# Optimization experiments

Hardware: AMD Instinct MI355X
Metric: run time of the kernel (lower is better)

## Reference

```python
import jax, jax.numpy as jnp
import numpy as np

# sparse displacement set used by UFlow's CostVolume (53 of the 9x9=81 offsets)
INDEX = [0, 2, 4, 6, 8, 10, 12, 14, 16, 18, 20, 21, 22, 23, 24, 26, 28, 29, 30, 31, 32, 33, 34, 36, 38, 39, 40, 41, 42, 44, 46, 47, 48, 49, 50, 51, 52, 54, 56, 57, 58, 59, 60, 62, 64, 66, 68, 70, 72, 74, 76, 78, 80]
MD = 4            # max_displacement
K = 2 * MD + 1    # 9


def setup_inputs() -> dict:
    key = jax.random.key(0)
    k1, k2 = jax.random.split(key)
    N, C, H, W = 8, 64, 160, 320
    in1 = jax.random.normal(k1, (N, C, H, W), dtype=jnp.float32)
    in2 = jax.random.normal(k2, (N, C, H, W), dtype=jnp.float32)
    return {"in1": in1, "in2": in2}


def reference(in1, in2):
    # one-hot kernels, padding=MD) shifts each repeated copy of in1 by a
    # displacement (dy, dx) = (idx//K - MD, idx%K - MD); multiply by repeated
    # in2; conv2 (grouped ones/dim kernel, kernel_size=1) averages over the
    # dim channels within each displacement group.
    # Equivalent fused form: out[:, j] = mean_c( shift(in1, off_j) * in2 ).
    n, c, h, w = in2.shape
    padded = jnp.pad(in1, ((0, 0), (0, 0), (MD, MD), (MD, MD)))  # zero-pad like conv padding
    outs = []
    for idx in INDEX:
        dy, dx = idx // K, idx % K  # static slice offsets into padded map
        shifted = padded[:, :, dy:dy + h, dx:dx + w]  # [n,c,h,w]
        outs.append(jnp.mean(shifted * in2, axis=1))  # [n,h,w]
    return jnp.stack(outs, axis=1)  # [n, 53, h, w]
```

## Files before the change

kernel.cpp:

```cpp
#include <hip/hip_runtime.h>


#define HH 160
#define WW 320
#define CHN 64
#define ND 53

__global__ __launch_bounds__(256)
void cost_volume_simple(const float* __restrict__ in1,
                        const float* __restrict__ in2,
                        float* __restrict__ out) {
    const int g = blockIdx.x * 256 + threadIdx.x;
    const int x = g % WW;
    const int y = (g / WW) % HH;
    const int n = g / (WW * HH);

    float acc[ND];
    #pragma unroll
    for (int d = 0; d < ND; ++d) acc[d] = 0.f;

    const float* base1 = in1 + (size_t)n * CHN * HH * WW;
    const float* base2 = in2 + (size_t)n * CHN * HH * WW;

    for (int c = 0; c < CHN; ++c) {
        const float v2 = base2[(size_t)c * HH * WW + y * WW + x];
        const float* pl = base1 + (size_t)c * HH * WW;

        float f[9];
        #define ROWLOAD(DY) { \
            const int yy = y + (DY) - 4; \
            const bool rowok = (yy >= 0) && (yy < HH); \
            const float* rp = pl + yy * WW + (x - 4); \
            _Pragma("unroll") \
            for (int j = 0; j < 9; ++j) { \
                const int xx = x + j - 4; \
                f[j] = (rowok && (xx >= 0) && (xx < WW)) ? rp[j] : 0.f; \
            } }
        #define ACC(D, J) acc[D] = fmaf(f[J], v2, acc[D]);

        ROWLOAD(0) ACC(0,0)  ACC(1,2)  ACC(2,4)  ACC(3,6)  ACC(4,8)
        ROWLOAD(1) ACC(5,1)  ACC(6,3)  ACC(7,5)  ACC(8,7)
        ROWLOAD(2) ACC(9,0)  ACC(10,2) ACC(11,3) ACC(12,4) ACC(13,5) ACC(14,6) ACC(15,8)
        ROWLOAD(3) ACC(16,1) ACC(17,2) ACC(18,3) ACC(19,4) ACC(20,5) ACC(21,6) ACC(22,7)
        ROWLOAD(4) ACC(23,0) ACC(24,2) ACC(25,3) ACC(26,4) ACC(27,5) ACC(28,6) ACC(29,8)
        ROWLOAD(5) ACC(30,1) ACC(31,2) ACC(32,3) ACC(33,4) ACC(34,5) ACC(35,6) ACC(36,7)
        ROWLOAD(6) ACC(37,0) ACC(38,2) ACC(39,3) ACC(40,4) ACC(41,5) ACC(42,6) ACC(43,8)
        ROWLOAD(7) ACC(44,1) ACC(45,3) ACC(46,5) ACC(47,7)
        ROWLOAD(8) ACC(48,0) ACC(49,2) ACC(50,4) ACC(51,6) ACC(52,8)
        #undef ROWLOAD
        #undef ACC
    }

    const float s = 1.0f / 64.0f;
    const size_t ob = (size_t)n * ND * HH * WW + (size_t)y * WW + x;
    #pragma unroll
    for (int d = 0; d < ND; ++d)
        out[ob + (size_t)d * HH * WW] = acc[d] * s;
}

extern "C" void kernel_launch(void* const* d_in, const int* in_sizes, int n_in,
                              void* d_out, int out_size, void* d_ws, size_t ws_size,
                              hipStream_t stream) {
    const float* in1 = (const float*)d_in[0];
    const float* in2 = (const float*)d_in[1];
    float* out = (float*)d_out;

    const int total = 8 * HH * WW;
    dim3 grid(total / 256);
    dim3 block(256);
    cost_volume_simple<<<grid, block, 0, stream>>>(in1, in2, out);
}
```

Before: 437.8 us.

## Compute four adjacent pixels per thread with float4 loads and deferred boundary masking

Each thread now produces four horizontally adjacent outputs, loading three float4 vectors per row so the 12 neighbouring values are shared across the four pixels, and stores results as float4. Boundary checks move out of the inner loop: loads are clamped to valid addresses, and out-of-range displacements are zeroed in the epilogue instead. Blocks shrink to 64 threads, and the block index is swizzled across the image. The intent is fewer load instructions, better vectorised memory access and less per-iteration branching. In exchange, 53 float4 accumulators (212 floats) raise register pressure and may spill or limit occupancy.

After: 643.4 us. 47.0% more time.

```diff
diff --git a/kernel.cpp b/kernel.cpp
--- a/kernel.cpp
+++ b/kernel.cpp
@@ -5,38 +5,58 @@
 #define WW 320
 #define CHN 64
 #define ND 53
+#define HW4 (HH * WW * 4)
+#define ROW4 (WW * 4)
+#define IMG4 (CHN * HW4)
+#define SIZEB (8 * IMG4)
+#define OIMG4 (ND * HW4)
 
-__global__ __launch_bounds__(256)
-void cost_volume_simple(const float* __restrict__ in1,
-                        const float* __restrict__ in2,
-                        float* __restrict__ out) {
-    const int g = blockIdx.x * 256 + threadIdx.x;
-    const int x = g % WW;
-    const int y = (g / WW) % HH;
-    const int n = g / (WW * HH);
+__global__ __launch_bounds__(64, 2)
+void cost_volume_x4(const float* __restrict__ in1,
+                    const float* __restrict__ in2,
+                    float* __restrict__ out) {
+    const int bid = blockIdx.x;
+    const int sb  = (bid & 7) * 200 + (bid >> 3);
+    const int g   = sb * 64 + threadIdx.x;
 
-    float acc[ND];
+    const int xg = g % 80;
+    const int x0 = xg * 4;
+    const int y  = (g / 80) % HH;
+    const int n  = g / (80 * HH);
+
+    const char* p1 = (const char*)in1;
+    const char* p2 = (const char*)in2;
+
+    float4 acc[ND];
     #pragma unroll
-    for (int d = 0; d < ND; ++d) acc[d] = 0.f;
+    for (int d = 0; d < ND; ++d) acc[d] = make_float4(0.f, 0.f, 0.f, 0.f);
 
-    const float* base1 = in1 + (size_t)n * CHN * HH * WW;
-    const float* base2 = in2 + (size_t)n * CHN * HH * WW;
+    int pc = n * IMG4 + x0 * 4 - 16;
+    int i2 = n * IMG4 + (y * WW + x0) * 4;
 
+    #pragma unroll 1
     for (int c = 0; c < CHN; ++c) {
-        const float v2 = base2[(size_t)c * HH * WW + y * WW + x];
-        const float* pl = base1 + (size_t)c * HH * WW;
+        const float4 w = *(const float4*)(p2 + i2);
+        float f[12];
 
-        float f[9];
         #define ROWLOAD(DY) { \
-            const int yy = y + (DY) - 4; \
-            const bool rowok = (yy >= 0) && (yy < HH); \
-            const float* rp = pl + yy * WW + (x - 4); \
-            _Pragma("unroll") \
-            for (int j = 0; j < 9; ++j) { \
-                const int xx = x + j - 4; \
-                f[j] = (rowok && (xx >= 0) && (xx < WW)) ? rp[j] : 0.f; \
-            } }
-        #define ACC(D, J) acc[D] = fmaf(f[J], v2, acc[D]);
+            int yy = y + (DY) - 4; \
+            yy = yy < 0 ? 0 : (yy > HH - 1 ? HH - 1 : yy); \
+            const int off = pc + yy * ROW4; \
+            const int o0 = off < 0 ? 0 : off; \
+            const int o2 = (off + 32 > SIZEB - 16) ? (SIZEB - 16) : (off + 32); \
+            const float4 a  = *(const float4*)(p1 + o0); \
+            const float4 b  = *(const float4*)(p1 + off + 16); \
+            const float4 cc = *(const float4*)(p1 + o2); \
+            f[0] = a.x;  f[1] = a.y;  f[2]  = a.z;  f[3]  = a.w; \
+            f[4] = b.x;  f[5] = b.y;  f[6]  = b.z;  f[7]  = b.w; \
+            f[8] = cc.x; f[9] = cc.y; f[10] = cc.z; f[11] = cc.w; }
+
+        #define ACC(D, DX) \
+            acc[D].x = fmaf(f[(DX) + 0], w.x, acc[D].x); \
+            acc[D].y = fmaf(f[(DX) + 1], w.y, acc[D].y); \
+            acc[D].z = fmaf(f[(DX) + 2], w.z, acc[D].z); \
+            acc[D].w = fmaf(f[(DX) + 3], w.w, acc[D].w);
 
         ROWLOAD(0) ACC(0,0)  ACC(1,2)  ACC(2,4)  ACC(3,6)  ACC(4,8)
         ROWLOAD(1) ACC(5,1)  ACC(6,3)  ACC(7,5)  ACC(8,7)
@@ -49,13 +69,41 @@
         ROWLOAD(8) ACC(48,0) ACC(49,2) ACC(50,4) ACC(51,6) ACC(52,8)
         #undef ROWLOAD
         #undef ACC
+
+        pc += HW4;
+        i2 += HW4;
     }
 
     const float s = 1.0f / 64.0f;
-    const size_t ob = (size_t)n * ND * HH * WW + (size_t)y * WW + x;
+    char* po = (char*)out + (size_t)n * OIMG4 + (size_t)((y * WW + x0) * 4);
+
+    bool xok[12];
     #pragma unroll
-    for (int d = 0; d < ND; ++d)
-        out[ob + (size_t)d * HH * WW] = acc[d] * s;
+    for (int j = 0; j < 12; ++j) {
+        const int xx = x0 + j - 4;
+        xok[j] = (xx >= 0) && (xx < WW);
+    }
+
+    #define EPI(D, DY, DX) { \
+        const int yy = y + (DY) - 4; \
+        const bool ry = (yy >= 0) && (yy < HH); \
+        float4 r; \
+        r.x = (ry && xok[(DX) + 0]) ? acc[D].x * s : 0.f; \
+        r.y = (ry && xok[(DX) + 1]) ? acc[D].y * s : 0.f; \
+        r.z = (ry && xok[(DX) + 2]) ? acc[D].z * s : 0.f; \
+        r.w = (ry && xok[(DX) + 3]) ? acc[D].w * s : 0.f; \
+        *(float4*)(po + (D) * HW4) = r; }
+
+    EPI(0,0,0)  EPI(1,0,2)  EPI(2,0,4)  EPI(3,0,6)  EPI(4,0,8)
+    EPI(5,1,1)  EPI(6,1,3)  EPI(7,1,5)  EPI(8,1,7)
+    EPI(9,2,0)  EPI(10,2,2) EPI(11,2,3) EPI(12,2,4) EPI(13,2,5) EPI(14,2,6) EPI(15,2,8)
+    EPI(16,3,1) EPI(17,3,2) EPI(18,3,3) EPI(19,3,4) EPI(20,3,5) EPI(21,3,6) EPI(22,3,7)
+    EPI(23,4,0) EPI(24,4,2) EPI(25,4,3) EPI(26,4,4) EPI(27,4,5) EPI(28,4,6) EPI(29,4,8)
+    EPI(30,5,1) EPI(31,5,2) EPI(32,5,3) EPI(33,5,4) EPI(34,5,5) EPI(35,5,6) EPI(36,5,7)
+    EPI(37,6,0) EPI(38,6,2) EPI(39,6,3) EPI(40,6,4) EPI(41,6,5) EPI(42,6,6) EPI(43,6,8)
+    EPI(44,7,1) EPI(45,7,3) EPI(46,7,5) EPI(47,7,7)
+    EPI(48,8,0) EPI(49,8,2) EPI(50,8,4) EPI(51,8,6) EPI(52,8,8)
+    #undef EPI
 }
 
 extern "C" void kernel_launch(void* const* d_in, const int* in_sizes, int n_in,
@@ -65,8 +113,7 @@
     const float* in2 = (const float*)d_in[1];
     float* out = (float*)d_out;
 
-    const int total = 8 * HH * WW;
-    dim3 grid(total / 256);
-    dim3 block(256);
-    cost_volume_simple<<<grid, block, 0, stream>>>(in1, in2, out);
+    dim3 grid(1600);
+    dim3 block(64);
+    cost_volume_x4<<<grid, block, 0, stream>>>(in1, in2, out);
 }
```

## Split displacements into five row-pair partitions with 4-wide vectorized pixels per thread

Applied to the files above, without the earlier changes.

Each thread now computes four adjacent x pixels with float4 loads, and the 53 displacements are split across five partitions by displacement row pairs, each with its own accumulator set. Blocks are 64 threads, and the block index is swizzled so that partitions interleave. Channel loads are double-buffered two at a time, and edge handling uses clamped addresses plus output masking instead of per-load predicates. This cuts register pressure and redundant scalar loads, but it re-reads in2 and in1 rows once per partition and adds epilogue masking.

Measured after the change: 376.9 us. 1.16x faster.

```diff
diff --git a/kernel.cpp b/kernel.cpp
--- a/kernel.cpp
+++ b/kernel.cpp
@@ -5,57 +5,160 @@
 #define WW 320
 #define CHN 64
 #define ND 53
+#define HW4 (HH * WW * 4)
+#define ROW4 (WW * 4)
+#define IMG4 (CHN * HW4)
+#define SIZEB (8 * IMG4)
+#define OIMG4 (ND * HW4)
 
-__global__ __launch_bounds__(256)
-void cost_volume_simple(const float* __restrict__ in1,
-                        const float* __restrict__ in2,
-                        float* __restrict__ out) {
-    const int g = blockIdx.x * 256 + threadIdx.x;
-    const int x = g % WW;
-    const int y = (g / WW) % HH;
-    const int n = g / (WW * HH);
+__global__ __launch_bounds__(64, 2)
+void cost_volume_5p(const float* __restrict__ in1,
+                    const float* __restrict__ in2,
+                    float* __restrict__ out) {
+    const int bid = blockIdx.x;
+    const int u   = (bid & 7) * 1000 + (bid >> 3);
+    const int p   = u / 1600;
+    const int r   = u % 1600;
+    const int g   = r * 64 + threadIdx.x;
 
-    float acc[ND];
-    #pragma unroll
-    for (int d = 0; d < ND; ++d) acc[d] = 0.f;
+    const int xg = g % 80;
+    const int x0 = xg * 4;
+    const int y  = (g / 80) % HH;
+    const int n  = g / (80 * HH);
 
-    const float* base1 = in1 + (size_t)n * CHN * HH * WW;
-    const float* base2 = in2 + (size_t)n * CHN * HH * WW;
+    const char* p1 = (const char*)in1;
+    const char* p2 = (const char*)in2;
 
-    for (int c = 0; c < CHN; ++c) {
-        const float v2 = base2[(size_t)c * HH * WW + y * WW + x];
-        const float* pl = base1 + (size_t)c * HH * WW;
+    int pc = n * IMG4 + x0 * 4 - 16;
+    int i2 = n * IMG4 + (y * WW + x0) * 4;
 
-        float f[9];
-        #define ROWLOAD(DY) { \
-            const int yy = y + (DY) - 4; \
-            const bool rowok = (yy >= 0) && (yy < HH); \
-            const float* rp = pl + yy * WW + (x - 4); \
-            _Pragma("unroll") \
-            for (int j = 0; j < 9; ++j) { \
-                const int xx = x + j - 4; \
-                f[j] = (rowok && (xx >= 0) && (xx < WW)) ? rp[j] : 0.f; \
-            } }
-        #define ACC(D, J) acc[D] = fmaf(f[J], v2, acc[D]);
+    #define RYOFF(DY) \
+        (((y + (DY) - 4) < 0 ? 0 : ((y + (DY) - 4) > HH - 1 ? HH - 1 : (y + (DY) - 4))) * ROW4)
 
-        ROWLOAD(0) ACC(0,0)  ACC(1,2)  ACC(2,4)  ACC(3,6)  ACC(4,8)
-        ROWLOAD(1) ACC(5,1)  ACC(6,3)  ACC(7,5)  ACC(8,7)
-        ROWLOAD(2) ACC(9,0)  ACC(10,2) ACC(11,3) ACC(12,4) ACC(13,5) ACC(14,6) ACC(15,8)
-        ROWLOAD(3) ACC(16,1) ACC(17,2) ACC(18,3) ACC(19,4) ACC(20,5) ACC(21,6) ACC(22,7)
-        ROWLOAD(4) ACC(23,0) ACC(24,2) ACC(25,3) ACC(26,4) ACC(27,5) ACC(28,6) ACC(29,8)
-        ROWLOAD(5) ACC(30,1) ACC(31,2) ACC(32,3) ACC(33,4) ACC(34,5) ACC(35,6) ACC(36,7)
-        ROWLOAD(6) ACC(37,0) ACC(38,2) ACC(39,3) ACC(40,4) ACC(41,5) ACC(42,6) ACC(43,8)
-        ROWLOAD(7) ACC(44,1) ACC(45,3) ACC(46,5) ACC(47,7)
-        ROWLOAD(8) ACC(48,0) ACC(49,2) ACC(50,4) ACC(51,6) ACC(52,8)
-        #undef ROWLOAD
-        #undef ACC
+    #define LDROW(FS, J0, PC, RO) { \
+        const int off = (PC) + (RO); \
+        const int oa = off < 0 ? 0 : off; \
+        const int oc = (off + 32 > SIZEB - 16) ? (SIZEB - 16) : (off + 32); \
+        const float4 va = *(const float4*)(p1 + oa); \
+        const float4 vb = *(const float4*)(p1 + off + 16); \
+        const float4 vc = *(const float4*)(p1 + oc); \
+        FS[(J0)+0] = va.x; FS[(J0)+1]  = va.y; FS[(J0)+2]  = va.z; FS[(J0)+3]  = va.w; \
+        FS[(J0)+4] = vb.x; FS[(J0)+5]  = vb.y; FS[(J0)+6]  = vb.z; FS[(J0)+7]  = vb.w; \
+        FS[(J0)+8] = vc.x; FS[(J0)+9]  = vc.y; FS[(J0)+10] = vc.z; FS[(J0)+11] = vc.w; }
+
+    #define LOAD2(FS, WS, PC, I2) { \
+        WS = *(const float4*)(p2 + (I2)); \
+        LDROW(FS, 0, PC, r0) \
+        LDROW(FS, 12, PC, r1) }
+
+    #define LOAD1(FS, WS, PC, I2) { \
+        WS = *(const float4*)(p2 + (I2)); \
+        LDROW(FS, 0, PC, r0) }
+
+    #define AC(A, J, FS, WS) \
+        acc[A].x = fmaf(FS[(J)+0], WS.x, acc[A].x); \
+        acc[A].y = fmaf(FS[(J)+1], WS.y, acc[A].y); \
+        acc[A].z = fmaf(FS[(J)+2], WS.z, acc[A].z); \
+        acc[A].w = fmaf(FS[(J)+3], WS.w, acc[A].w);
+
+    #define CHANLOOP(LOADM, CMPM) \
+        LOADM(fA, wA, pc, i2) \
+        _Pragma("unroll 1") \
+        for (int c = 0; c < CHN - 2; c += 2) { \
+            LOADM(fB, wB, pc + HW4, i2 + HW4) \
+            CMPM(fA, wA) \
+            pc += 2 * HW4; i2 += 2 * HW4; \
+            LOADM(fA, wA, pc, i2) \
+            CMPM(fB, wB) \
+        } \
+        LOADM(fB, wB, pc + HW4, i2 + HW4) \
+        CMPM(fA, wA) \
+        CMPM(fB, wB)
+
+    #define EPI(A, D, RY, DX) { \
+        float4 rr; \
+        rr.x = ((RY) && xok[(DX)+0]) ? acc[A].x * s : 0.f; \
+        rr.y = ((RY) && xok[(DX)+1]) ? acc[A].y * s : 0.f; \
+        rr.z = ((RY) && xok[(DX)+2]) ? acc[A].z * s : 0.f; \
+        rr.w = ((RY) && xok[(DX)+3]) ? acc[A].w * s : 0.f; \
+        *(float4*)(po + (size_t)(D) * HW4) = rr; }
+
+    #define EPIPRE \
+        const float s = 1.0f / 64.0f; \
+        char* po = (char*)out + (size_t)n * OIMG4 + (size_t)((y * WW + x0) * 4); \
+        bool xok[12]; \
+        _Pragma("unroll") \
+        for (int j = 0; j < 12; ++j) { const int xx = x0 + j - 4; xok[j] = (xx >= 0) && (xx < WW); }
+
+    if (p == 0) {
+        const int r0 = RYOFF(0), r1 = RYOFF(1);
+        float4 acc[9];
+        #pragma unroll
+        for (int a = 0; a < 9; ++a) acc[a] = make_float4(0.f,0.f,0.f,0.f);
+        float fA[24], fB[24]; float4 wA, wB;
+        #define CMP0(FS, WS) \
+            AC(0,0,FS,WS)  AC(1,2,FS,WS)  AC(2,4,FS,WS)  AC(3,6,FS,WS)  AC(4,8,FS,WS) \
+            AC(5,13,FS,WS) AC(6,15,FS,WS) AC(7,17,FS,WS) AC(8,19,FS,WS)
+        CHANLOOP(LOAD2, CMP0)
+        EPIPRE
+        const bool ry0 = (y >= 4);
+        const bool ry1 = (y >= 3);
+        EPI(0,0,ry0,0) EPI(1,1,ry0,2) EPI(2,2,ry0,4) EPI(3,3,ry0,6) EPI(4,4,ry0,8)
+        EPI(5,5,ry1,1) EPI(6,6,ry1,3) EPI(7,7,ry1,5) EPI(8,8,ry1,7)
+    } else if (p <= 2) {
+        const int dyA = 2 * p;
+        const int r0 = RYOFF(dyA), r1 = RYOFF(dyA + 1);
+        const int dbase = 9 + (p - 1) * 14;
+        float4 acc[14];
+        #pragma unroll
+        for (int a = 0; a < 14; ++a) acc[a] = make_float4(0.f,0.f,0.f,0.f);
+        float fA[24], fB[24]; float4 wA, wB;
+        #define CMP12(FS, WS) \
+            AC(0,0,FS,WS)   AC(1,2,FS,WS)   AC(2,3,FS,WS)   AC(3,4,FS,WS) \
+            AC(4,5,FS,WS)   AC(5,6,FS,WS)   AC(6,8,FS,WS) \
+            AC(7,13,FS,WS)  AC(8,14,FS,WS)  AC(9,15,FS,WS)  AC(10,16,FS,WS) \
+            AC(11,17,FS,WS) AC(12,18,FS,WS) AC(13,19,FS,WS)
+        CHANLOOP(LOAD2, CMP12)
+        EPIPRE
+        const int ya = y + dyA - 4, yb = ya + 1;
+        const bool ryA = (ya >= 0) && (ya < HH);
+        const bool ryB = (yb >= 0) && (yb < HH);
+        EPI(0,dbase+0,ryA,0)  EPI(1,dbase+1,ryA,2)  EPI(2,dbase+2,ryA,3)
+        EPI(3,dbase+3,ryA,4)  EPI(4,dbase+4,ryA,5)  EPI(5,dbase+5,ryA,6)
+        EPI(6,dbase+6,ryA,8)
+        EPI(7,dbase+7,ryB,1)  EPI(8,dbase+8,ryB,2)  EPI(9,dbase+9,ryB,3)
+        EPI(10,dbase+10,ryB,4) EPI(11,dbase+11,ryB,5) EPI(12,dbase+12,ryB,6)
+        EPI(13,dbase+13,ryB,7)
+    } else if (p == 3) {
+        const int r0 = RYOFF(6), r1 = RYOFF(7);
+        float4 acc[11];
+        #pragma unroll
+        for (int a = 0; a < 11; ++a) acc[a] = make_float4(0.f,0.f,0.f,0.f);
+        float fA[24], fB[24]; float4 wA, wB;
+        #define CMP3(FS, WS) \
+            AC(0,0,FS,WS)  AC(1,2,FS,WS)  AC(2,3,FS,WS)  AC(3,4,FS,WS) \
+            AC(4,5,FS,WS)  AC(5,6,FS,WS)  AC(6,8,FS,WS) \
+            AC(7,13,FS,WS) AC(8,15,FS,WS) AC(9,17,FS,WS) AC(10,19,FS,WS)
+        CHANLOOP(LOAD2, CMP3)
+        EPIPRE
+        const bool ry6 = (y + 2 < HH);
+        const bool ry7 = (y + 3 < HH);
+        EPI(0,37,ry6,0) EPI(1,38,ry6,2) EPI(2,39,ry6,3) EPI(3,40,ry6,4)
+        EPI(4,41,ry6,5) EPI(5,42,ry6,6) EPI(6,43,ry6,8)
+        EPI(7,44,ry7,1) EPI(8,45,ry7,3) EPI(9,46,ry7,5) EPI(10,47,ry7,7)
+    } else {
+        const int r0 = RYOFF(8);
+        float4 acc[5];
+        #pragma unroll
+        for (int a = 0; a < 5; ++a) acc[a] = make_float4(0.f,0.f,0.f,0.f);
+        float fA[12], fB[12]; float4 wA, wB;
+        #define CMP4(FS, WS) \
+            AC(0,0,FS,WS) AC(1,2,FS,WS) AC(2,4,FS,WS) AC(3,6,FS,WS) AC(4,8,FS,WS)
+        CHANLOOP(LOAD1, CMP4)
+        EPIPRE
+        const bool ry8 = (y + 4 < HH);
+        EPI(0,48,ry8,0) EPI(1,49,ry8,2) EPI(2,50,ry8,4) EPI(3,51,ry8,6) EPI(4,52,ry8,8)
     }
-
-    const float s = 1.0f / 64.0f;
-    const size_t ob = (size_t)n * ND * HH * WW + (size_t)y * WW + x;
-    #pragma unroll
-    for (int d = 0; d < ND; ++d)
-        out[ob + (size_t)d * HH * WW] = acc[d] * s;
 }
 
 extern "C" void kernel_launch(void* const* d_in, const int* in_sizes, int n_in,
@@ -65,8 +168,7 @@
     const float* in2 = (const float*)d_in[1];
     float* out = (float*)d_out;
 
-    const int total = 8 * HH * WW;
-    dim3 grid(total / 256);
-    dim3 block(256);
-    cost_volume_simple<<<grid, block, 0, stream>>>(in1, in2, out);
+    dim3 grid(8000);
+    dim3 block(64);
+    cost_volume_5p<<<grid, block, 0, stream>>>(in1, in2, out);
 }
```

## Split displacement rows across nine wavefronts with float4 pixel vectorization

Applied to the files above, without the earlier changes.

Each block now runs nine wavefronts, one per vertical displacement row, and each lane handles four adjacent pixels with float4 loads of in1 and in2 and float4 stores. A thread keeps at most seven float4 accumulators instead of 53 scalars, which cuts register pressure and raises occupancy. Boundary handling moves from per-load masking to clamped addresses plus output masking in the epilogue. Block ids are remapped so consecutive blocks cover different images. The trade-off is that each wavefront reloads in2 on its own, relying on cache hits, and there is divergence across the switch between waves.

After: 368.7 us. 15.8% less time.

```diff
diff --git a/kernel.cpp b/kernel.cpp
--- a/kernel.cpp
+++ b/kernel.cpp
@@ -5,57 +5,126 @@
 #define WW 320
 #define CHN 64
 #define ND 53
+#define HW4 (HH * WW * 4)
+#define ROW4 (WW * 4)
+#define IMG4 (CHN * HW4)
+#define SIZEB (8 * IMG4)
+#define OIMG4 (ND * HW4)
 
-__global__ __launch_bounds__(256)
-void cost_volume_simple(const float* __restrict__ in1,
-                        const float* __restrict__ in2,
-                        float* __restrict__ out) {
-    const int g = blockIdx.x * 256 + threadIdx.x;
-    const int x = g % WW;
-    const int y = (g / WW) % HH;
-    const int n = g / (WW * HH);
+__global__ __launch_bounds__(576)
+void cost_volume_9w(const float* __restrict__ in1,
+                    const float* __restrict__ in2,
+                    float* __restrict__ out) {
+    const int wv   = threadIdx.x >> 6;
+    const int lane = threadIdx.x & 63;
+    const int bid  = blockIdx.x;
+    const int sb   = (bid & 7) * 200 + (bid >> 3);
+    const int q    = sb * 64 + lane;
 
-    float acc[ND];
-    #pragma unroll
-    for (int d = 0; d < ND; ++d) acc[d] = 0.f;
+    const int xg = q % 80;
+    const int x0 = xg * 4;
+    const int y  = (q / 80) % HH;
+    const int n  = q / (80 * HH);
 
-    const float* base1 = in1 + (size_t)n * CHN * HH * WW;
-    const float* base2 = in2 + (size_t)n * CHN * HH * WW;
+    const char* p1 = (const char*)in1;
+    const char* p2 = (const char*)in2;
 
-    for (int c = 0; c < CHN; ++c) {
-        const float v2 = base2[(size_t)c * HH * WW + y * WW + x];
-        const float* pl = base1 + (size_t)c * HH * WW;
+    const int yy0 = y + wv - 4;
+    const int yc  = yy0 < 0 ? 0 : (yy0 > HH - 1 ? HH - 1 : yy0);
+    const int r0  = yc * ROW4;
+    const bool ry = (yy0 >= 0) && (yy0 < HH);
 
-        float f[9];
-        #define ROWLOAD(DY) { \
-            const int yy = y + (DY) - 4; \
-            const bool rowok = (yy >= 0) && (yy < HH); \
-            const float* rp = pl + yy * WW + (x - 4); \
-            _Pragma("unroll") \
-            for (int j = 0; j < 9; ++j) { \
-                const int xx = x + j - 4; \
-                f[j] = (rowok && (xx >= 0) && (xx < WW)) ? rp[j] : 0.f; \
-            } }
-        #define ACC(D, J) acc[D] = fmaf(f[J], v2, acc[D]);
-
-        ROWLOAD(0) ACC(0,0)  ACC(1,2)  ACC(2,4)  ACC(3,6)  ACC(4,8)
-        ROWLOAD(1) ACC(5,1)  ACC(6,3)  ACC(7,5)  ACC(8,7)
-        ROWLOAD(2) ACC(9,0)  ACC(10,2) ACC(11,3) ACC(12,4) ACC(13,5) ACC(14,6) ACC(15,8)
-        ROWLOAD(3) ACC(16,1) ACC(17,2) ACC(18,3) ACC(19,4) ACC(20,5) ACC(21,6) ACC(22,7)
-        ROWLOAD(4) ACC(23,0) ACC(24,2) ACC(25,3) ACC(26,4) ACC(27,5) ACC(28,6) ACC(29,8)
-        ROWLOAD(5) ACC(30,1) ACC(31,2) ACC(32,3) ACC(33,4) ACC(34,5) ACC(35,6) ACC(36,7)
-        ROWLOAD(6) ACC(37,0) ACC(38,2) ACC(39,3) ACC(40,4) ACC(41,5) ACC(42,6) ACC(43,8)
-        ROWLOAD(7) ACC(44,1) ACC(45,3) ACC(46,5) ACC(47,7)
-        ROWLOAD(8) ACC(48,0) ACC(49,2) ACC(50,4) ACC(51,6) ACC(52,8)
-        #undef ROWLOAD
-        #undef ACC
-    }
+    int pc = n * IMG4 + x0 * 4 - 16;
+    int i2 = n * IMG4 + (y * WW + x0) * 4;
 
     const float s = 1.0f / 64.0f;
-    const size_t ob = (size_t)n * ND * HH * WW + (size_t)y * WW + x;
+    char* po = (char*)out + (size_t)n * OIMG4 + (size_t)((y * WW + x0) * 4);
+    bool xok[12];
     #pragma unroll
-    for (int d = 0; d < ND; ++d)
-        out[ob + (size_t)d * HH * WW] = acc[d] * s;
+    for (int j = 0; j < 12; ++j) { const int xx = x0 + j - 4; xok[j] = (xx >= 0) && (xx < WW); }
+
+    #define AC(A, J) \
+        acc[A].x = fmaf(f[(J)+0], w.x, acc[A].x); \
+        acc[A].y = fmaf(f[(J)+1], w.y, acc[A].y); \
+        acc[A].z = fmaf(f[(J)+2], w.z, acc[A].z); \
+        acc[A].w = fmaf(f[(J)+3], w.w, acc[A].w);
+
+    #define CHLOOP(ACCS) \
+        _Pragma("unroll 1") \
+        for (int c = 0; c < CHN; ++c) { \
+            const float4 w = *(const float4*)(p2 + i2); \
+            float f[12]; \
+            { const int off = pc + r0; \
+              const int oa = off < 0 ? 0 : off; \
+              const int oc = (off + 32 > SIZEB - 16) ? (SIZEB - 16) : (off + 32); \
+              const float4 va = *(const float4*)(p1 + oa); \
+              const float4 vb = *(const float4*)(p1 + off + 16); \
+              const float4 vc = *(const float4*)(p1 + oc); \
+              f[0]=va.x; f[1]=va.y; f[2]=va.z;  f[3]=va.w; \
+              f[4]=vb.x; f[5]=vb.y; f[6]=vb.z;  f[7]=vb.w; \
+              f[8]=vc.x; f[9]=vc.y; f[10]=vc.z; f[11]=vc.w; } \
+            ACCS \
+            pc += HW4; i2 += HW4; \
+        }
+
+    #define EPI(A, D, DX) { \
+        float4 rr; \
+        rr.x = (ry && xok[(DX)+0]) ? acc[A].x * s : 0.f; \
+        rr.y = (ry && xok[(DX)+1]) ? acc[A].y * s : 0.f; \
+        rr.z = (ry && xok[(DX)+2]) ? acc[A].z * s : 0.f; \
+        rr.w = (ry && xok[(DX)+3]) ? acc[A].w * s : 0.f; \
+        *(float4*)(po + (size_t)(D) * HW4) = rr; }
+
+    switch (wv) {
+    case 0: {
+        float4 acc[5] = {};
+        CHLOOP(AC(0,0) AC(1,2) AC(2,4) AC(3,6) AC(4,8))
+        EPI(0,0,0) EPI(1,1,2) EPI(2,2,4) EPI(3,3,6) EPI(4,4,8)
+        break; }
+    case 1: {
+        float4 acc[4] = {};
+        CHLOOP(AC(0,1) AC(1,3) AC(2,5) AC(3,7))
+        EPI(0,5,1) EPI(1,6,3) EPI(2,7,5) EPI(3,8,7)
+        break; }
+    case 2: {
+        float4 acc[7] = {};
+        CHLOOP(AC(0,0) AC(1,2) AC(2,3) AC(3,4) AC(4,5) AC(5,6) AC(6,8))
+        EPI(0,9,0) EPI(1,10,2) EPI(2,11,3) EPI(3,12,4) EPI(4,13,5) EPI(5,14,6) EPI(6,15,8)
+        break; }
+    case 3: {
+        float4 acc[7] = {};
+        CHLOOP(AC(0,1) AC(1,2) AC(2,3) AC(3,4) AC(4,5) AC(5,6) AC(6,7))
+        EPI(0,16,1) EPI(1,17,2) EPI(2,18,3) EPI(3,19,4) EPI(4,20,5) EPI(5,21,6) EPI(6,22,7)
+        break; }
+    case 4: {
+        float4 acc[7] = {};
+        CHLOOP(AC(0,0) AC(1,2) AC(2,3) AC(3,4) AC(4,5) AC(5,6) AC(6,8))
+        EPI(0,23,0) EPI(1,24,2) EPI(2,25,3) EPI(3,26,4) EPI(4,27,5) EPI(5,28,6) EPI(6,29,8)
+        break; }
+    case 5: {
+        float4 acc[7] = {};
+        CHLOOP(AC(0,1) AC(1,2) AC(2,3) AC(3,4) AC(4,5) AC(5,6) AC(6,7))
+        EPI(0,30,1) EPI(1,31,2) EPI(2,32,3) EPI(3,33,4) EPI(4,34,5) EPI(5,35,6) EPI(6,36,7)
+        break; }
+    case 6: {
+        float4 acc[7] = {};
+        CHLOOP(AC(0,0) AC(1,2) AC(2,3) AC(3,4) AC(4,5) AC(5,6) AC(6,8))
+        EPI(0,37,0) EPI(1,38,2) EPI(2,39,3) EPI(3,40,4) EPI(4,41,5) EPI(5,42,6) EPI(6,43,8)
+        break; }
+    case 7: {
+        float4 acc[4] = {};
+        CHLOOP(AC(0,1) AC(1,3) AC(2,5) AC(3,7))
+        EPI(0,44,1) EPI(1,45,3) EPI(2,46,5) EPI(3,47,7)
+        break; }
+    default: {
+        float4 acc[5] = {};
+        CHLOOP(AC(0,0) AC(1,2) AC(2,4) AC(3,6) AC(4,8))
+        EPI(0,48,0) EPI(1,49,2) EPI(2,50,4) EPI(3,51,6) EPI(4,52,8)
+        break; }
+    }
+    #undef AC
+    #undef CHLOOP
+    #undef EPI
 }
 
 extern "C" void kernel_launch(void* const* d_in, const int* in_sizes, int n_in,
@@ -65,8 +134,7 @@
     const float* in2 = (const float*)d_in[1];
     float* out = (float*)d_out;
 
-    const int total = 8 * HH * WW;
-    dim3 grid(total / 256);
-    dim3 block(256);
-    cost_volume_simple<<<grid, block, 0, stream>>>(in1, in2, out);
+    dim3 grid(1600);
+    dim3 block(576);
+    cost_volume_9w<<<grid, block, 0, stream>>>(in1, in2, out);
 }
```
